# Optimization experiments

Hardware: AMD Instinct MI355X
Metric: run time of the kernel (lower is better)

Reference implementation:

```python
import math
import jax, jax.numpy as jnp
import numpy as np

B, N = 1, 512
C_S, C_Z, C_H, H, PQ, PV = 384, 128, 16, 12, 4, 8
CONCAT = H * C_Z + H * C_H + H * PV * 3 + H * PV  # 2112
W_C = math.sqrt(2.0 / (9.0 * PQ))
W_L = math.sqrt(1.0 / 3.0)


def setup_inputs() -> dict:
    key = jax.random.key(0)
    ks = jax.random.split(key, 16)
    sc = 0.02
    return {
        "s": jax.random.normal(ks[0], (B, N, C_S), jnp.float32),
        "z": jax.random.normal(ks[1], (B, N, N, C_Z), jnp.float32),
        "R": jax.random.normal(ks[2], (B, N, 3, 3), jnp.float32),
        "t": jax.random.normal(ks[3], (B, N, 3), jnp.float32),
        "mask": jnp.ones((B, N), dtype=bool),
        "Wqkv": jax.random.normal(ks[4], (C_S, 3 * H * C_H), jnp.float32) * sc,
        "Wqk_pts": jax.random.normal(ks[5], (C_S, 2 * H * PQ * 3), jnp.float32) * sc,
        "bqk_pts": jnp.zeros((2 * H * PQ * 3,), jnp.float32),
        "Wv_pts": jax.random.normal(ks[6], (C_S, H * PV * 3), jnp.float32) * sc,
        "bv_pts": jnp.zeros((H * PV * 3,), jnp.float32),
        "Wb": jax.random.normal(ks[7], (C_Z, H), jnp.float32) * sc,
        "bb": jnp.zeros((H,), jnp.float32),
        "gamma": jnp.full((H,), 0.541324854612918, jnp.float32),
        "Wfin": jax.random.normal(ks[8], (CONCAT, C_S), jnp.float32) * sc,
        "bfin": jnp.zeros((C_S,), jnp.float32),
    }


def _apply_rigid(R, t, pts):
    # R: [B,N,3,3], t: [B,N,3], pts: [B,N,H,P,3] -> global frame
    return jnp.einsum('bnxy,bnhpy->bnhpx', R, pts) + t[:, :, None, None, :]


def _invert_apply_rigid(R, t, pts):
    # R^T (pts - t)
    return jnp.einsum('bnyx,bnhpy->bnhpx', R, pts - t[:, :, None, None, :])


def reference(s, z, R, t, mask, Wqkv, Wqk_pts, bqk_pts, Wv_pts, bv_pts,
              Wb, bb, gamma, Wfin, bfin):
    b_, n_ = s.shape[0], s.shape[1]
    qkv = (s @ Wqkv).reshape(b_, n_, 3, H, C_H)
    q, k, v = qkv[:, :, 0], qkv[:, :, 1], qkv[:, :, 2]
    term1 = jnp.einsum('bihc,bjhc->bhij', q, k) / math.sqrt(C_H)
    term2 = jnp.transpose(z @ Wb + bb, (0, 3, 1, 2))  # [B,H,i,j]

    qk_pts = (s @ Wqk_pts + bqk_pts).reshape(b_, n_, 2, H, PQ, 3)
    q_pts, k_pts = qk_pts[:, :, 0], qk_pts[:, :, 1]
    qg = _apply_rigid(R, t, q_pts)  # [B,N,H,PQ,3]
    kg = _apply_rigid(R, t, k_pts)
    # squared distance summed over points and xyz -> [B,i,j,H]
    diff2 = jnp.sum((qg[:, :, None] - kg[:, None]) ** 2, axis=(-2, -1))
    term3 = (jax.nn.softplus(gamma)[None, :, None, None] * (W_C / 2.0)
             * jnp.transpose(diff2, (0, 3, 1, 2)))

    logits = W_L * (term1 + term2 - term3)
    logits = jnp.where(mask[:, None, None, :], logits, -1e9)
    aw = jax.nn.softmax(logits, axis=-1)  # [B,H,i,j]

    out_tilde = jnp.einsum('bhij,bijc->bihc', aw, z)
    out = jnp.einsum('bhij,bjhc->bihc', aw, v)

    v_pts = (s @ Wv_pts + bv_pts).reshape(b_, n_, H, PV, 3)
    vg = _apply_rigid(R, t, v_pts)
    o_global = jnp.einsum('bhij,bjhvx->bihvx', aw, vg)
    o_vec = _invert_apply_rigid(R, t, o_global)  # [B,N,H,PV,3]
    o_norm = jnp.sqrt(jnp.sum(o_vec ** 2, axis=-1) + 1e-8)

    feats = jnp.concatenate([
        out_tilde.reshape(b_, n_, -1),
        out.reshape(b_, n_, -1),
        o_vec.reshape(b_, n_, -1),
        o_norm.reshape(b_, n_, -1),
    ], axis=-1)
    return feats @ Wfin + bfin
```

## Files before the change

### kernel.cpp

```cpp
#include <hip/hip_runtime.h>
#include <math.h>

#define NSEQ 512
#define CS   384
#define NH   12
#define CHD  16
#define CZ   128
#define CONCATD 2112

#define W_L      0.57735026918962576f
#define W_C_HALF 0.117851130197757925f

typedef float f32x4 __attribute__((ext_vector_type(4)));
typedef short bf16x8 __attribute__((ext_vector_type(8)));
typedef unsigned int u32x2 __attribute__((ext_vector_type(2)));
typedef unsigned int u32x4 __attribute__((ext_vector_type(4)));

__device__ __forceinline__ unsigned short f2bf(float f) {
    union { float f; unsigned int u; } v; v.f = f;
    unsigned int u = v.u + 0x7FFFu + ((v.u >> 16) & 1u);
    return (unsigned short)(u >> 16);
}
__device__ __forceinline__ float bf2f(unsigned short u) {
    union { unsigned int i; float f; } v; v.i = ((unsigned int)u) << 16; return v.f;
}

#define MFMA16(A, B, C) __builtin_amdgcn_mfma_f32_16x16x32_bf16((A), (B), (C), 0, 0, 0)

#define RAWBAR() do {                                          \
    __builtin_amdgcn_sched_barrier(0);                         \
    asm volatile("s_waitcnt lgkmcnt(0)" ::: "memory");         \
    __builtin_amdgcn_s_barrier();                              \
    __builtin_amdgcn_sched_barrier(0);                         \
} while (0)

__global__ __launch_bounds__(256) void ipa_prep(
    const float* __restrict__ s, const float* __restrict__ Wqkv,
    const float* __restrict__ Wqk, const float* __restrict__ Wv,
    const float* __restrict__ bqk, const float* __restrict__ bv,
    const float* __restrict__ Wfin,
    unsigned short* __restrict__ sb, unsigned short* __restrict__ WcatT,
    float* __restrict__ biasv, unsigned short* __restrict__ WfinT)
{
    __shared__ float tile[32][33];
    if (blockIdx.x >= 314) {
        int b = blockIdx.x - 314;
        int kt = b / 12, nt = b - kt * 12;
        int k0 = kt * 32, n0 = nt * 32;
        #pragma unroll
        for (int it = 0; it < 4; ++it) {
            int idx = it * 256 + threadIdx.x;
            int ty = idx >> 5, tx = idx & 31;
            tile[ty][tx] = Wfin[(size_t)(k0 + ty) * 384 + n0 + tx];
        }
        __syncthreads();
        #pragma unroll
        for (int it = 0; it < 4; ++it) {
            int idx = it * 256 + threadIdx.x;
            int ty = idx >> 5, tx = idx & 31;
            WfinT[(size_t)(n0 + ty) * 2112 + k0 + tx] = f2bf(tile[tx][ty]);
        }
        return;
    }
    int v = blockIdx.x * 256 + threadIdx.x;
    if (v < 24576) {
        const float* src = s + (size_t)v * 8;
        f32x4 a = *(const f32x4*)src, b = *(const f32x4*)(src + 4);
        u32x4 pk;
        pk[0] = (unsigned)f2bf(a[0]) | ((unsigned)f2bf(a[1]) << 16);
        pk[1] = (unsigned)f2bf(a[2]) | ((unsigned)f2bf(a[3]) << 16);
        pk[2] = (unsigned)f2bf(b[0]) | ((unsigned)f2bf(b[1]) << 16);
        pk[3] = (unsigned)f2bf(b[2]) | ((unsigned)f2bf(b[3]) << 16);
        *(u32x4*)(sb + (size_t)v * 8) = pk;
    } else if (v < 79872) {
        int v2 = v - 24576;
        int n = v2 / 48;
        int kq = (v2 - n * 48) * 8;
        const float* W; int stride; int col; float sc = 1.f;
        if (n < 576)      { W = Wqkv; stride = 576; col = n;       if (n < 192) sc = 0.25f; }
        else if (n < 864) { W = Wqk;  stride = 288; col = n - 576; }
        else              { W = Wv;   stride = 288; col = n - 864; }
        const float* src = W + (size_t)kq * stride + col;
        unsigned int pk[4];
        #pragma unroll
        for (int e = 0; e < 4; ++e) {
            float v0 = src[(size_t)(2 * e) * stride] * sc;
            float v1 = src[(size_t)(2 * e + 1) * stride] * sc;
            pk[e] = (unsigned)f2bf(v0) | ((unsigned)f2bf(v1) << 16);
        }
        u32x4 pkv = {pk[0], pk[1], pk[2], pk[3]};
        *(u32x4*)(WcatT + (size_t)n * 384 + kq) = pkv;
    } else if (v < 80160) {
        int c0 = (v - 79872) * 4;
        #pragma unroll
        for (int e = 0; e < 4; ++e) {
            int c = c0 + e;
            biasv[c] = (c < 576) ? 0.f : ((c < 864) ? bqk[c - 576] : bv[c - 864]);
        }
    }
}

__global__ __launch_bounds__(256) void ipa_pg_t2(
    const unsigned short* __restrict__ sb, const unsigned short* __restrict__ WcatT,
    const float* __restrict__ biasv, float* __restrict__ proj,
    const float* __restrict__ z, const float* __restrict__ Wb,
    const float* __restrict__ bb, unsigned short* __restrict__ S)
{
    __shared__ __align__(16) char smem[26112];
    const int tid = threadIdx.x, lane = tid & 63, wv = tid >> 6;
    const int l15 = lane & 15, hi = lane >> 4;
    const int koff = hi * 8;
    const f32x4 ZV = {0.f, 0.f, 0.f, 0.f};

    if (blockIdx.x < 288) {
        const int n0 = ((int)blockIdx.x % 18) * 64;
        const int m0 = ((int)blockIdx.x / 18) * 32;
        unsigned short (*A_l)[136] = (unsigned short(*)[136])smem;
        unsigned short (*B_l)[136] = (unsigned short(*)[136])(smem + 8704);
        f32x4 C[4];
        #pragma unroll
        for (int nf = 0; nf < 4; ++nf) C[nf] = ZV;

        #pragma unroll
        for (int kc = 0; kc < 3; ++kc) {
            const int k0 = kc * 128;
            __syncthreads();
            #pragma unroll
            for (int it = 0; it < 2; ++it) {
                int v = it * 256 + tid;
                int row = v >> 4, c8 = v & 15;
                *(u32x4*)&A_l[row][c8 * 8] =
                    *(const u32x4*)(sb + (size_t)(m0 + row) * 384 + k0 + c8 * 8);
            }
            #pragma unroll
            for (int it = 0; it < 4; ++it) {
                int v = it * 256 + tid;
                int row = v >> 4, c8 = v & 15;
                *(u32x4*)&B_l[row][c8 * 8] =
                    *(const u32x4*)(WcatT + (size_t)(n0 + row) * 384 + k0 + c8 * 8);
            }
            __syncthreads();
            if (wv < 2) {
                #pragma unroll
                for (int ks = 0; ks < 4; ++ks) {
                    bf16x8 Af = *(const bf16x8*)&A_l[wv * 16 + l15][ks * 32 + koff];
                    #pragma unroll
                    for (int nf = 0; nf < 4; ++nf) {
                        bf16x8 Bf = *(const bf16x8*)&B_l[nf * 16 + l15][ks * 32 + koff];
                        C[nf] = MFMA16(Af, Bf, C[nf]);
                    }
                }
            }
        }
        if (wv < 2) {
            #pragma unroll
            for (int nf = 0; nf < 4; ++nf) {
                int col = n0 + nf * 16 + l15;
                float bval = biasv[col];
                #pragma unroll
                for (int r = 0; r < 4; ++r) {
                    int row = m0 + wv * 16 + hi * 4 + r;
                    proj[(size_t)row * 1152 + col] = C[nf][r] + bval;
                }
            }
        }
    } else {
        const int b = blockIdx.x - 288;
        const int i = b >> 3;
        const int j0 = (b & 7) * 64;
        unsigned short (*z_l)[136] = (unsigned short(*)[136])smem;

        bf16x8 wbf[4];
        #pragma unroll
        for (int ks = 0; ks < 4; ++ks) {
            bf16x8 rfr;
            #pragma unroll
            for (int e = 0; e < 8; ++e) {
                int c = ks * 32 + koff + e;
                float w = (l15 < 12) ? Wb[c * 12 + l15] : 0.f;
                rfr[e] = (short)f2bf(w);
            }
            wbf[ks] = rfr;
        }
        float bbv[4];
        #pragma unroll
        for (int r = 0; r < 4; ++r) { int h = hi * 4 + r; bbv[r] = (h < 12) ? bb[h] : 0.f; }

        #pragma unroll
        for (int it = 0; it < 4; ++it) {
            int u = it * 256 + tid;
            int row = u >> 4, c8 = u & 15;
            const float* src = z + ((size_t)(i * 512 + j0 + row)) * 128 + c8 * 8;
            f32x4 a = *(const f32x4*)src, bq = *(const f32x4*)(src + 4);
            u32x4 pk;
            pk[0] = (unsigned)f2bf(a[0]) | ((unsigned)f2bf(a[1]) << 16);
            pk[1] = (unsigned)f2bf(a[2]) | ((unsigned)f2bf(a[3]) << 16);
            pk[2] = (unsigned)f2bf(bq[0]) | ((unsigned)f2bf(bq[1]) << 16);
            pk[3] = (unsigned)f2bf(bq[2]) | ((unsigned)f2bf(bq[3]) << 16);
            *(u32x4*)&z_l[row][c8 * 8] = pk;
        }
        __syncthreads();

        const int jcol = wv * 16 + l15;
        f32x4 C = ZV;
        #pragma unroll
        for (int ks = 0; ks < 4; ++ks)
            C = MFMA16(wbf[ks], *(const bf16x8*)&z_l[jcol][ks * 32 + koff], C);
        #pragma unroll
        for (int r = 0; r < 4; ++r) {
            int h = hi * 4 + r;
            if (h < 12)
                S[(size_t)h * 262144 + (size_t)i * 512 + j0 + jcol] = f2bf(C[r] + bbv[r]);
        }
    }
}

__global__ __launch_bounds__(256) void ipa_projep(
    const float* __restrict__ proj, const float* __restrict__ R, const float* __restrict__ t,
    const float* __restrict__ gamma,
    unsigned short* __restrict__ Aaug, unsigned short* __restrict__ Baug,
    unsigned short* __restrict__ VcatT, float* __restrict__ rq, float* __restrict__ rk)
{
    const int half = threadIdx.x >> 7;
    const int i = blockIdx.x * 2 + half;
    const int st = threadIdx.x & 127;
    __shared__ float R_l[2][9], t_l[2][3], sq_l[2][96];
    __shared__ float sh_l[12];

    if (st < 9) R_l[half][st] = R[i * 9 + st];
    if (st >= 12 && st < 15) t_l[half][st - 12] = t[i * 3 + st - 12];
    if (threadIdx.x >= 240 && threadIdx.x < 252) {
        int h = threadIdx.x - 240;
        float spg = logf(1.f + __expf(gamma[h])) * W_C_HALF;
        sh_l[h] = sqrtf(2.f * spg);
    }
    __syncthreads();

    const float* row = proj + (size_t)i * 1152;

    for (int c = st; c < 576; c += 128) {
        unsigned short b16 = f2bf(row[c]);
        if (c < 192) {
            Aaug[((size_t)(c >> 4) * 512 + i) * 32 + (c & 15)] = b16;
        } else if (c < 384) {
            int cc = c - 192;
            Baug[((size_t)(cc >> 4) * 512 + i) * 32 + (cc & 15)] = b16;
        } else {
            int cc = c - 384;
            VcatT[((size_t)((cc >> 4) * 48 + (cc & 15))) * 512 + i] = b16;
        }
    }

    const float* Rr = R_l[half];
    const float* tt = t_l[half];
    for (int pt = st; pt < 192; pt += 128) {
        if (pt < 96) {
            int lp = (pt < 48) ? pt : pt - 48;
            int h = lp >> 2, p = lp & 3;
            int base = 576 + pt * 3;
            float p0 = row[base], p1 = row[base + 1], p2 = row[base + 2];
            float sh = sh_l[h];
            float g0 = (Rr[0] * p0 + Rr[1] * p1 + Rr[2] * p2 + tt[0]) * sh;
            float g1 = (Rr[3] * p0 + Rr[4] * p1 + Rr[5] * p2 + tt[1]) * sh;
            float g2 = (Rr[6] * p0 + Rr[7] * p1 + Rr[8] * p2 + tt[2]) * sh;
            sq_l[half][pt] = g0 * g0 + g1 * g1 + g2 * g2;
            unsigned short* dst =
                (pt < 48 ? Aaug : Baug) + ((size_t)h * 512 + i) * 32 + 16 + p * 3;
            dst[0] = f2bf(g0); dst[1] = f2bf(g1); dst[2] = f2bf(g2);
        } else {
            int vp = pt - 96;
            int h = vp >> 3, vv = vp & 7;
            int base = 864 + vp * 3;
            float p0 = row[base], p1 = row[base + 1], p2 = row[base + 2];
            float g0 = Rr[0] * p0 + Rr[1] * p1 + Rr[2] * p2 + tt[0];
            float g1 = Rr[3] * p0 + Rr[4] * p1 + Rr[5] * p2 + tt[1];
            float g2 = Rr[6] * p0 + Rr[7] * p1 + Rr[8] * p2 + tt[2];
            size_t rbase = ((size_t)h * 48 + 16 + vv * 3) * 512 + i;
            VcatT[rbase] = f2bf(g0);
            VcatT[rbase + 512] = f2bf(g1);
            VcatT[rbase + 1024] = f2bf(g2);
        }
    }
    __syncthreads();

    if (st < 24) {
        int qk = st / 12, h = st - qk * 12;
        int b0 = qk * 48 + h * 4;
        float ssum = sq_l[half][b0] + sq_l[half][b0 + 1]
                   + sq_l[half][b0 + 2] + sq_l[half][b0 + 3];
        (qk ? rk : rq)[h * 512 + i] = 0.5f * ssum;
    }
    if (st >= 32 && st < 56) {
        int e = st - 32;
        int mt = e / 12, h = e - mt * 12;
        *(unsigned long long*)((mt ? Baug : Aaug) + ((size_t)h * 512 + i) * 32 + 28) = 0ull;
    }
}

__global__ __launch_bounds__(256) void ipa_smax(
    const unsigned short* __restrict__ S, const unsigned short* __restrict__ Aaug,
    const unsigned short* __restrict__ Baug, const float* __restrict__ rq,
    const float* __restrict__ rk, unsigned short* __restrict__ P1, float* __restrict__ l1)
{
    const int h = blockIdx.x, i0 = blockIdx.y * 16;
    const int tid = threadIdx.x, lane = tid & 63, wv = tid >> 6;
    const int col = lane & 15, hi = lane >> 4;
    __shared__ __align__(16) unsigned short Baug_l[512][40];
    __shared__ __align__(16) unsigned short Aaug_l[16][40];
    __shared__ float rk_l[512], rq_l[16];
    __shared__ float pmx[4][16], psm[4][16];

    for (int u = tid; u < 2048; u += 256) {
        int row = u >> 2, seg = u & 3;
        *(u32x4*)&Baug_l[row][seg * 8] =
            *(const u32x4*)(Baug + ((size_t)h * 512 + row) * 32 + seg * 8);
    }
    if (tid < 64) {
        int row = tid >> 2, seg = tid & 3;
        *(u32x4*)&Aaug_l[row][seg * 8] =
            *(const u32x4*)(Aaug + ((size_t)h * 512 + i0 + row) * 32 + seg * 8);
    }
    for (int u = tid; u < 512; u += 256) rk_l[u] = rk[h * 512 + u];
    if (tid >= 64 && tid < 80) rq_l[tid - 64] = rq[h * 512 + i0 + tid - 64];
    __syncthreads();

    const f32x4 ZV = {0.f, 0.f, 0.f, 0.f};
    bf16x8 Af = *(const bf16x8*)&Aaug_l[col][hi * 8];
    f32x4 C[8];
    #pragma unroll
    for (int nf = 0; nf < 8; ++nf) {
        int n = wv * 8 + nf;
        bf16x8 Bf = *(const bf16x8*)&Baug_l[n * 16 + col][hi * 8];
        C[nf] = MFMA16(Af, Bf, ZV);
    }
    const unsigned short* Srow = S + (size_t)h * 262144 + (size_t)i0 * 512;
    float rmax[4] = {-1e30f, -1e30f, -1e30f, -1e30f};
    #pragma unroll
    for (int nf = 0; nf < 8; ++nf) {
        int j = wv * 128 + nf * 16 + col;
        float rkj = rk_l[j];
        #pragma unroll
        for (int r = 0; r < 4; ++r) {
            int il = hi * 4 + r;
            float Sv = bf2f(Srow[(size_t)il * 512 + j]);
            float L = W_L * (C[nf][r] + Sv - rq_l[il] - rkj);
            C[nf][r] = L;
            rmax[r] = fmaxf(rmax[r], L);
        }
    }
    #pragma unroll
    for (int o = 8; o; o >>= 1)
        #pragma unroll
        for (int r = 0; r < 4; ++r) rmax[r] = fmaxf(rmax[r], __shfl_xor(rmax[r], o));
    if (col == 0)
        #pragma unroll
        for (int r = 0; r < 4; ++r) pmx[wv][hi * 4 + r] = rmax[r];
    __syncthreads();
    float M[4], lsum[4] = {0.f, 0.f, 0.f, 0.f};
    #pragma unroll
    for (int r = 0; r < 4; ++r) {
        int il = hi * 4 + r;
        M[r] = fmaxf(fmaxf(pmx[0][il], pmx[1][il]), fmaxf(pmx[2][il], pmx[3][il]));
    }
    #pragma unroll
    for (int nf = 0; nf < 8; ++nf)
        #pragma unroll
        for (int r = 0; r < 4; ++r) {
            float p = __expf(C[nf][r] - M[r]);
            C[nf][r] = p;
            lsum[r] += p;
        }
    #pragma unroll
    for (int o = 8; o; o >>= 1)
        #pragma unroll
        for (int r = 0; r < 4; ++r) lsum[r] += __shfl_xor(lsum[r], o);
    if (col == 0)
        #pragma unroll
        for (int r = 0; r < 4; ++r) psm[wv][hi * 4 + r] = lsum[r];
    __syncthreads();
    if (wv == 0 && col == 0) {
        #pragma unroll
        for (int r = 0; r < 4; ++r) {
            int il = hi * 4 + r;
            l1[h * 512 + i0 + il] = psm[0][il] + psm[1][il] + psm[2][il] + psm[3][il];
        }
    }
    unsigned short* Prow = P1 + (size_t)h * 262144 + (size_t)i0 * 512;
    #pragma unroll
    for (int nf = 0; nf < 8; ++nf) {
        int j = wv * 128 + nf * 16 + col;
        #pragma unroll
        for (int r = 0; r < 4; ++r)
            Prow[(size_t)(hi * 4 + r) * 512 + j] = f2bf(C[nf][r]);
    }
}

__global__ __launch_bounds__(256) void ipa_otpv(
    const float* __restrict__ z, const unsigned short* __restrict__ P1,
    const float* __restrict__ l1, const unsigned short* __restrict__ VcatT,
    const float* __restrict__ R, const float* __restrict__ t,
    unsigned short* __restrict__ featsb)
{
    __shared__ __align__(16) char smem[35072];
    const int tid = threadIdx.x, lane = tid & 63, wv = tid >> 6;
    const int l15 = lane & 15, hi = lane >> 4;
    const int koff = hi * 8;
    const f32x4 ZV = {0.f, 0.f, 0.f, 0.f};

    if (blockIdx.x < 1024) {
        const int i = blockIdx.x >> 1;
        const int chalf = ((int)blockIdx.x & 1) * 64;
        unsigned short (*P_l)[520] = (unsigned short(*)[520])smem;
        typedef unsigned short zt_t[64][72];
        zt_t* zT = (zt_t*)(smem + 16640);

        for (int u = tid; u < 1024; u += 256) {
            int row = u >> 6, c8 = u & 63;
            *(u32x4*)&P_l[row][c8 * 8] =
                *(const u32x4*)(P1 + (size_t)row * 262144 + (size_t)i * 512 + c8 * 8);
        }
        __syncthreads();

        f32x4 sa[4];
        #pragma unroll
        for (int it = 0; it < 4; ++it) {
            int u = it * 256 + tid;
            int jj = u >> 4, c4l = u & 15;
            sa[it] = *(const f32x4*)(z + ((size_t)(i * 512 + jj)) * 128 + chalf + c4l * 4);
        }

        f32x4 Co = ZV;
        for (int jt = 0; jt < 8; ++jt) {
            const int cur = jt & 1;
            #pragma unroll
            for (int it = 0; it < 4; ++it) {
                int u = it * 256 + tid;
                int jj = u >> 4, c4l = u & 15;
                f32x4 zv = sa[it];
                unsigned short b0 = f2bf(zv[0]), b1 = f2bf(zv[1]), b2 = f2bf(zv[2]), b3 = f2bf(zv[3]);
                unsigned int w01 = (unsigned)b0 | ((unsigned)b1 << 16);
                unsigned int w23 = (unsigned)b2 | ((unsigned)b3 << 16);
                unsigned int p01 = (unsigned int)__shfl_xor((int)w01, 16);
                unsigned int p23 = (unsigned int)__shfl_xor((int)w23, 16);
                bool even = ((tid & 16) == 0);
                unsigned short q0 = (unsigned short)(p01 & 0xffff), q1 = (unsigned short)(p01 >> 16);
                unsigned short q2 = (unsigned short)(p23 & 0xffff), q3 = (unsigned short)(p23 >> 16);
                unsigned int w0, w1, w2, w3;
                if (even) {
                    w0 = (unsigned)b0 | ((unsigned)q0 << 16); w1 = (unsigned)b1 | ((unsigned)q1 << 16);
                    w2 = (unsigned)b2 | ((unsigned)q2 << 16); w3 = (unsigned)b3 | ((unsigned)q3 << 16);
                } else {
                    w0 = (unsigned)q0 | ((unsigned)b0 << 16); w1 = (unsigned)q1 | ((unsigned)b1 << 16);
                    w2 = (unsigned)q2 | ((unsigned)b2 << 16); w3 = (unsigned)q3 | ((unsigned)b3 << 16);
                }
                int jp = jj >> 1;
                int rot = ((c4l >> 1) & 3) + (even ? 0 : 2);
                #pragma unroll
                for (int ss = 0; ss < 2; ++ss) {
                    int rr = (rot + ss) & 3;
                    unsigned int val = (rr == 0) ? w0 : ((rr == 1) ? w1 : ((rr == 2) ? w2 : w3));
                    *(unsigned int*)&zT[cur][4 * c4l + rr][2 * jp] = val;
                }
            }
            if (jt < 7) {
                const int j0n = (jt + 1) * 64;
                #pragma unroll
                for (int it = 0; it < 4; ++it) {
                    int u = it * 256 + tid;
                    int jj = u >> 4, c4l = u & 15;
                    sa[it] = *(const f32x4*)(z + ((size_t)(i * 512 + j0n + jj)) * 128 + chalf + c4l * 4);
                }
            }
            RAWBAR();
            #pragma unroll
            for (int ks2 = 0; ks2 < 2; ++ks2) {
                bf16x8 Af = *(const bf16x8*)&P_l[l15][jt * 64 + ks2 * 32 + koff];
                bf16x8 Bf = *(const bf16x8*)&zT[cur][wv * 16 + l15][ks2 * 32 + koff];
                Co = MFMA16(Af, Bf, Co);
            }
        }

        #pragma unroll
        for (int r = 0; r < 4; ++r) {
            int h = hi * 4 + r;
            if (h < 12)
                featsb[(size_t)i * CONCATD + h * 128 + chalf + wv * 16 + l15]
                    = f2bf(Co[r] / l1[h * 512 + i]);
        }
    } else {
        const int b = blockIdx.x - 1024;
        const int h = b >> 3, i0 = (b & 7) * 64;
        const int col = l15;
        unsigned short (*V_l)[264] = (unsigned short(*)[264])smem;
        float (*ogl)[26] = (float(*)[26])(smem + 25344);

        f32x4 C0 = ZV, C1 = ZV, C2 = ZV;
        const unsigned short* Pbase =
            P1 + (size_t)h * 262144 + (size_t)(i0 + wv * 16 + col) * 512;
        #pragma unroll
        for (int hf = 0; hf < 2; ++hf) {
            __syncthreads();
            for (int u = tid; u < 1536; u += 256) {
                int row = u >> 5, c8 = u & 31;
                *(u32x4*)&V_l[row][c8 * 8] =
                    *(const u32x4*)(VcatT + ((size_t)h * 48 + row) * 512 + hf * 256 + c8 * 8);
            }
            __syncthreads();
            #pragma unroll
            for (int ks2 = 0; ks2 < 8; ++ks2) {
                bf16x8 Af = *(const bf16x8*)(Pbase + hf * 256 + ks2 * 32 + hi * 8);
                C0 = MFMA16(Af, *(const bf16x8*)&V_l[col][ks2 * 32 + hi * 8],      C0);
                C1 = MFMA16(Af, *(const bf16x8*)&V_l[16 + col][ks2 * 32 + hi * 8], C1);
                C2 = MFMA16(Af, *(const bf16x8*)&V_l[32 + col][ks2 * 32 + hi * 8], C2);
            }
        }
        #pragma unroll
        for (int r = 0; r < 4; ++r) {
            int il = wv * 16 + hi * 4 + r;
            int irow = i0 + il;
            float inv = 1.f / l1[h * 512 + irow];
            featsb[(size_t)irow * CONCATD + 1536 + h * 16 + col] = f2bf(C0[r] * inv);
            ogl[il][col] = C1[r] * inv;
            if (col < 8) ogl[il][16 + col] = C2[r] * inv;
        }
        __syncthreads();

        #pragma unroll
        for (int it = 0; it < 2; ++it) {
            int item = it * 256 + tid;
            int il = item >> 3, v = item & 7;
            int i = i0 + il;
            const float* Rr = R + i * 9;
            const float* tt = t + i * 3;
            float g0 = ogl[il][v * 3 + 0] - tt[0];
            float g1 = ogl[il][v * 3 + 1] - tt[1];
            float g2 = ogl[il][v * 3 + 2] - tt[2];
            float o0 = Rr[0] * g0 + Rr[3] * g1 + Rr[6] * g2;
            float o1 = Rr[1] * g0 + Rr[4] * g1 + Rr[7] * g2;
            float o2 = Rr[2] * g0 + Rr[5] * g1 + Rr[8] * g2;
            unsigned short* frow = featsb + (size_t)i * CONCATD;
            frow[1728 + h * 24 + v * 3 + 0] = f2bf(o0);
            frow[1728 + h * 24 + v * 3 + 1] = f2bf(o1);
            frow[1728 + h * 24 + v * 3 + 2] = f2bf(o2);
            frow[2016 + h * 8 + v] = f2bf(sqrtf(o0 * o0 + o1 * o1 + o2 * o2 + 1e-8f));
        }
    }
}

__global__ __launch_bounds__(128) void ipa_finalb(
    const unsigned short* __restrict__ featsb, const unsigned short* __restrict__ WfinT,
    float* __restrict__ fpart)
{
    const int n0 = blockIdx.x * 64, m0 = blockIdx.y * 32;
    const int k0 = blockIdx.z * 192;
    const int tid = threadIdx.x, lane = tid & 63, wv = tid >> 6;
    const int l15 = lane & 15, hi = lane >> 4;
    __shared__ __align__(16) unsigned short A_l[32][200];
    __shared__ __align__(16) unsigned short B_l[64][200];

    #pragma unroll
    for (int it = 0; it < 6; ++it) {
        int v = it * 128 + tid;
        int row = v / 24, c8 = v % 24;
        *(u32x4*)&A_l[row][c8 * 8] =
            *(const u32x4*)(featsb + (size_t)(m0 + row) * CONCATD + k0 + c8 * 8);
    }
    #pragma unroll
    for (int it = 0; it < 12; ++it) {
        int v = it * 128 + tid;
        int row = v / 24, c8 = v % 24;
        *(u32x4*)&B_l[row][c8 * 8] =
            *(const u32x4*)(WfinT + (size_t)(n0 + row) * 2112 + k0 + c8 * 8);
    }
    __syncthreads();

    const f32x4 ZV = {0.f, 0.f, 0.f, 0.f};
    f32x4 C[4];
    #pragma unroll
    for (int nf = 0; nf < 4; ++nf) C[nf] = ZV;
    const int koff = hi * 8;
    #pragma unroll
    for (int ks = 0; ks < 6; ++ks) {
        bf16x8 Af = *(const bf16x8*)&A_l[wv * 16 + l15][ks * 32 + koff];
        #pragma unroll
        for (int nf = 0; nf < 4; ++nf) {
            bf16x8 Bf = *(const bf16x8*)&B_l[nf * 16 + l15][ks * 32 + koff];
            C[nf] = MFMA16(Af, Bf, C[nf]);
        }
    }
    float* P = fpart + (size_t)blockIdx.z * (NSEQ * CS);
    #pragma unroll
    for (int nf = 0; nf < 4; ++nf) {
        int colx = n0 + nf * 16 + l15;
        #pragma unroll
        for (int r = 0; r < 4; ++r) {
            int row = m0 + wv * 16 + hi * 4 + r;
            P[(size_t)row * CS + colx] = C[nf][r];
        }
    }
}

__global__ __launch_bounds__(256) void ipa_reduceb(
    const float* __restrict__ fpart, const float* __restrict__ bias, float* __restrict__ out)
{
    int idx = blockIdx.x * 256 + threadIdx.x;
    f32x4 acc = ((const f32x4*)bias)[idx % (CS / 4)];
    #pragma unroll
    for (int kc = 0; kc < 11; ++kc)
        acc += ((const f32x4*)(fpart + (size_t)kc * (NSEQ * CS)))[idx];
    ((f32x4*)out)[idx] = acc;
}

extern "C" void kernel_launch(void* const* d_in, const int* in_sizes, int n_in,
                              void* d_out, int out_size, void* d_ws, size_t ws_size,
                              hipStream_t stream) {
    (void)in_sizes; (void)n_in; (void)out_size; (void)ws_size;
    const float* s    = (const float*)d_in[0];
    const float* z    = (const float*)d_in[1];
    const float* R    = (const float*)d_in[2];
    const float* t    = (const float*)d_in[3];
    const float* Wqkv = (const float*)d_in[5];
    const float* Wqk  = (const float*)d_in[6];
    const float* bqk  = (const float*)d_in[7];
    const float* Wv   = (const float*)d_in[8];
    const float* bv   = (const float*)d_in[9];
    const float* Wb   = (const float*)d_in[10];
    const float* bb   = (const float*)d_in[11];
    const float* gam  = (const float*)d_in[12];
    const float* Wfin = (const float*)d_in[13];
    const float* bfin = (const float*)d_in[14];
    float* out = (float*)d_out;

    char* w8 = (char*)d_ws;
    unsigned short* S     = (unsigned short*)(w8 + 0);
    unsigned short* P1    = (unsigned short*)(w8 + 6291456);
    unsigned short* featsb= (unsigned short*)(w8 + 12582912);
    unsigned short* WfinT = (unsigned short*)(w8 + 14745600);
    unsigned short* Aaug  = (unsigned short*)(w8 + 16908288);
    unsigned short* Baug  = (unsigned short*)(w8 + 17301504);
    unsigned short* VcatT = (unsigned short*)(w8 + 17694720);
    float* rq             = (float*)(w8 + 18284544);
    float* rk             = (float*)(w8 + 18309120);
    float* l1             = (float*)(w8 + 18333696);
    float* fpart          = (float*)(w8 + 0);
    float* proj           = (float*)(w8 + 6291456 + 2359296);
    unsigned short* sb    = (unsigned short*)(w8 + 2359296);
    unsigned short* WcatT = (unsigned short*)(w8 + 2752512);
    float* biasv          = (float*)(w8 + 3637248);

    sb    = (unsigned short*)(w8 + 12582912);
    WcatT = (unsigned short*)(w8 + 12582912 + 393216);
    biasv = (float*)(w8 + 12582912 + 1277952);

    ipa_prep<<<1106, 256, 0, stream>>>(s, Wqkv, Wqk, Wv, bqk, bv, Wfin,
                                       sb, WcatT, biasv, WfinT);
    ipa_pg_t2<<<4384, 256, 0, stream>>>(sb, WcatT, biasv, proj, z, Wb, bb, S);
    ipa_projep<<<256, 256, 0, stream>>>(proj, R, t, gam, Aaug, Baug, VcatT, rq, rk);
    ipa_smax<<<dim3(12, 32), 256, 0, stream>>>(S, Aaug, Baug, rq, rk, P1, l1);
    ipa_otpv<<<1120, 256, 0, stream>>>(z, P1, l1, VcatT, R, t, featsb);
    ipa_finalb<<<dim3(6, 16, 11), 128, 0, stream>>>(featsb, WfinT, fpart);
    ipa_reduceb<<<192, 256, 0, stream>>>(fpart, bfin, out);
}
```

Baseline: 84.84 us.

## Fuse prep conversion kernel into projection/z-bias kernel, converting weights on the fly

Removes the separate prep launch by having the projection GEMM blocks convert s and the Wqkv/Wqk/Wv weights from fp32 to bf16 while loading tiles. The weight tile is transposed in registers with lane shuffles and stored into LDS. The bias is read directly from the inputs instead of a staged buffer. The Wfin transpose moves into the same launch as extra blocks. This saves one kernel launch and the intermediate global round-trip, at the cost of redundant fp32 loads and conversion work in each GEMM block.

```diff
diff --git a/kernel.cpp b/kernel.cpp
--- a/kernel.cpp
+++ b/kernel.cpp
@@ -34,77 +34,14 @@
     __builtin_amdgcn_sched_barrier(0);                         \
 } while (0)
 
-__global__ __launch_bounds__(256) void ipa_prep(
+__global__ __launch_bounds__(256) void ipa_l1(
+    const float* __restrict__ z, const float* __restrict__ Wb,
+    const float* __restrict__ bb, unsigned short* __restrict__ S,
     const float* __restrict__ s, const float* __restrict__ Wqkv,
     const float* __restrict__ Wqk, const float* __restrict__ Wv,
     const float* __restrict__ bqk, const float* __restrict__ bv,
-    const float* __restrict__ Wfin,
-    unsigned short* __restrict__ sb, unsigned short* __restrict__ WcatT,
-    float* __restrict__ biasv, unsigned short* __restrict__ WfinT)
-{
-    __shared__ float tile[32][33];
-    if (blockIdx.x >= 314) {
-        int b = blockIdx.x - 314;
-        int kt = b / 12, nt = b - kt * 12;
-        int k0 = kt * 32, n0 = nt * 32;
-        #pragma unroll
-        for (int it = 0; it < 4; ++it) {
-            int idx = it * 256 + threadIdx.x;
-            int ty = idx >> 5, tx = idx & 31;
-            tile[ty][tx] = Wfin[(size_t)(k0 + ty) * 384 + n0 + tx];
-        }
-        __syncthreads();
-        #pragma unroll
-        for (int it = 0; it < 4; ++it) {
-            int idx = it * 256 + threadIdx.x;
-            int ty = idx >> 5, tx = idx & 31;
-            WfinT[(size_t)(n0 + ty) * 2112 + k0 + tx] = f2bf(tile[tx][ty]);
-        }
-        return;
-    }
-    int v = blockIdx.x * 256 + threadIdx.x;
-    if (v < 24576) {
-        const float* src = s + (size_t)v * 8;
-        f32x4 a = *(const f32x4*)src, b = *(const f32x4*)(src + 4);
-        u32x4 pk;
-        pk[0] = (unsigned)f2bf(a[0]) | ((unsigned)f2bf(a[1]) << 16);
-        pk[1] = (unsigned)f2bf(a[2]) | ((unsigned)f2bf(a[3]) << 16);
-        pk[2] = (unsigned)f2bf(b[0]) | ((unsigned)f2bf(b[1]) << 16);
-        pk[3] = (unsigned)f2bf(b[2]) | ((unsigned)f2bf(b[3]) << 16);
-        *(u32x4*)(sb + (size_t)v * 8) = pk;
-    } else if (v < 79872) {
-        int v2 = v - 24576;
-        int n = v2 / 48;
-        int kq = (v2 - n * 48) * 8;
-        const float* W; int stride; int col; float sc = 1.f;
-        if (n < 576)      { W = Wqkv; stride = 576; col = n;       if (n < 192) sc = 0.25f; }
-        else if (n < 864) { W = Wqk;  stride = 288; col = n - 576; }
-        else              { W = Wv;   stride = 288; col = n - 864; }
-        const float* src = W + (size_t)kq * stride + col;
-        unsigned int pk[4];
-        #pragma unroll
-        for (int e = 0; e < 4; ++e) {
-            float v0 = src[(size_t)(2 * e) * stride] * sc;
-            float v1 = src[(size_t)(2 * e + 1) * stride] * sc;
-            pk[e] = (unsigned)f2bf(v0) | ((unsigned)f2bf(v1) << 16);
-        }
-        u32x4 pkv = {pk[0], pk[1], pk[2], pk[3]};
-        *(u32x4*)(WcatT + (size_t)n * 384 + kq) = pkv;
-    } else if (v < 80160) {
-        int c0 = (v - 79872) * 4;
-        #pragma unroll
-        for (int e = 0; e < 4; ++e) {
-            int c = c0 + e;
-            biasv[c] = (c < 576) ? 0.f : ((c < 864) ? bqk[c - 576] : bv[c - 864]);
-        }
-    }
-}
-
-__global__ __launch_bounds__(256) void ipa_pg_t2(
-    const unsigned short* __restrict__ sb, const unsigned short* __restrict__ WcatT,
-    const float* __restrict__ biasv, float* __restrict__ proj,
-    const float* __restrict__ z, const float* __restrict__ Wb,
-    const float* __restrict__ bb, unsigned short* __restrict__ S)
+    float* __restrict__ proj,
+    const float* __restrict__ Wfin, unsigned short* __restrict__ WfinT)
 {
     __shared__ __align__(16) char smem[26112];
     const int tid = threadIdx.x, lane = tid & 63, wv = tid >> 6;
@@ -112,9 +49,58 @@
     const int koff = hi * 8;
     const f32x4 ZV = {0.f, 0.f, 0.f, 0.f};
 
-    if (blockIdx.x < 288) {
-        const int n0 = ((int)blockIdx.x % 18) * 64;
-        const int m0 = ((int)blockIdx.x / 18) * 32;
+    if (blockIdx.x < 4096) {
+        const int b = blockIdx.x;
+        const int i = b >> 3;
+        const int j0 = (b & 7) * 64;
+        unsigned short (*z_l)[136] = (unsigned short(*)[136])smem;
+
+        bf16x8 wbf[4];
+        #pragma unroll
+        for (int ks = 0; ks < 4; ++ks) {
+            bf16x8 rfr;
+            #pragma unroll
+            for (int e = 0; e < 8; ++e) {
+                int c = ks * 32 + koff + e;
+                float w = (l15 < 12) ? Wb[c * 12 + l15] : 0.f;
+                rfr[e] = (short)f2bf(w);
+            }
+            wbf[ks] = rfr;
+        }
+        float bbv[4];
+        #pragma unroll
+        for (int r = 0; r < 4; ++r) { int h = hi * 4 + r; bbv[r] = (h < 12) ? bb[h] : 0.f; }
+
+        #pragma unroll
+        for (int it = 0; it < 4; ++it) {
+            int u = it * 256 + tid;
+            int row = u >> 4, c8 = u & 15;
+            const float* src = z + ((size_t)(i * 512 + j0 + row)) * 128 + c8 * 8;
+            f32x4 a = *(const f32x4*)src, bq = *(const f32x4*)(src + 4);
+            u32x4 pk;
+            pk[0] = (unsigned)f2bf(a[0]) | ((unsigned)f2bf(a[1]) << 16);
+            pk[1] = (unsigned)f2bf(a[2]) | ((unsigned)f2bf(a[3]) << 16);
+            pk[2] = (unsigned)f2bf(bq[0]) | ((unsigned)f2bf(bq[1]) << 16);
+            pk[3] = (unsigned)f2bf(bq[2]) | ((unsigned)f2bf(bq[3]) << 16);
+            *(u32x4*)&z_l[row][c8 * 8] = pk;
+        }
+        __syncthreads();
+
+        const int jcol = wv * 16 + l15;
+        f32x4 C = ZV;
+        #pragma unroll
+        for (int ks = 0; ks < 4; ++ks)
+            C = MFMA16(wbf[ks], *(const bf16x8*)&z_l[jcol][ks * 32 + koff], C);
+        #pragma unroll
+        for (int r = 0; r < 4; ++r) {
+            int h = hi * 4 + r;
+            if (h < 12)
+                S[(size_t)h * 262144 + (size_t)i * 512 + j0 + jcol] = f2bf(C[r] + bbv[r]);
+        }
+    } else if (blockIdx.x < 4384) {
+        const int b = blockIdx.x - 4096;
+        const int n0 = (b % 18) * 64;
+        const int m0 = (b / 18) * 32;
         unsigned short (*A_l)[136] = (unsigned short(*)[136])smem;
         unsigned short (*B_l)[136] = (unsigned short(*)[136])(smem + 8704);
         f32x4 C[4];
@@ -127,17 +113,57 @@
             __syncthreads();
             #pragma unroll
             for (int it = 0; it < 2; ++it) {
-                int v = it * 256 + tid;
-                int row = v >> 4, c8 = v & 15;
-                *(u32x4*)&A_l[row][c8 * 8] =
-                    *(const u32x4*)(sb + (size_t)(m0 + row) * 384 + k0 + c8 * 8);
+                int u = it * 256 + tid;
+                int row = u >> 4, c8 = u & 15;
+                const float* src = s + (size_t)(m0 + row) * 384 + k0 + c8 * 8;
+                f32x4 a = *(const f32x4*)src, bq = *(const f32x4*)(src + 4);
+                u32x4 pk;
+                pk[0] = (unsigned)f2bf(a[0]) | ((unsigned)f2bf(a[1]) << 16);
+                pk[1] = (unsigned)f2bf(a[2]) | ((unsigned)f2bf(a[3]) << 16);
+                pk[2] = (unsigned)f2bf(bq[0]) | ((unsigned)f2bf(bq[1]) << 16);
+                pk[3] = (unsigned)f2bf(bq[2]) | ((unsigned)f2bf(bq[3]) << 16);
+                *(u32x4*)&A_l[row][c8 * 8] = pk;
             }
             #pragma unroll
-            for (int it = 0; it < 4; ++it) {
-                int v = it * 256 + tid;
-                int row = v >> 4, c8 = v & 15;
-                *(u32x4*)&B_l[row][c8 * 8] =
-                    *(const u32x4*)(WcatT + (size_t)(n0 + row) * 384 + k0 + c8 * 8);
+            for (int kh = 0; kh < 2; ++kh) {
+                #pragma unroll
+                for (int it = 0; it < 4; ++it) {
+                    int u = it * 256 + tid;
+                    int kk = u >> 4, c4l = u & 15;
+                    int n = n0 + 4 * c4l;
+                    int k = k0 + kh * 64 + kk;
+                    const float* Wp; int ncols, coln; float sc = 1.f;
+                    if (n < 576)      { Wp = Wqkv; ncols = 576; coln = n;       if (n < 192) sc = 0.25f; }
+                    else if (n < 864) { Wp = Wqk;  ncols = 288; coln = n - 576; }
+                    else              { Wp = Wv;   ncols = 288; coln = n - 864; }
+                    f32x4 wval = *(const f32x4*)(Wp + (size_t)k * ncols + coln);
+                    wval *= sc;
+                    unsigned short b0 = f2bf(wval[0]), b1 = f2bf(wval[1]);
+                    unsigned short b2 = f2bf(wval[2]), b3 = f2bf(wval[3]);
+                    unsigned int w01 = (unsigned)b0 | ((unsigned)b1 << 16);
+                    unsigned int w23 = (unsigned)b2 | ((unsigned)b3 << 16);
+                    unsigned int p01 = (unsigned int)__shfl_xor((int)w01, 16);
+                    unsigned int p23 = (unsigned int)__shfl_xor((int)w23, 16);
+                    bool even = ((tid & 16) == 0);
+                    unsigned short q0 = (unsigned short)(p01 & 0xffff), q1 = (unsigned short)(p01 >> 16);
+                    unsigned short q2 = (unsigned short)(p23 & 0xffff), q3 = (unsigned short)(p23 >> 16);
+                    unsigned int w0, w1, w2, w3;
+                    if (even) {
+                        w0 = (unsigned)b0 | ((unsigned)q0 << 16); w1 = (unsigned)b1 | ((unsigned)q1 << 16);
+                        w2 = (unsigned)b2 | ((unsigned)q2 << 16); w3 = (unsigned)b3 | ((unsigned)q3 << 16);
+                    } else {
+                        w0 = (unsigned)q0 | ((unsigned)b0 << 16); w1 = (unsigned)q1 | ((unsigned)b1 << 16);
+                        w2 = (unsigned)q2 | ((unsigned)b2 << 16); w3 = (unsigned)q3 | ((unsigned)b3 << 16);
+                    }
+                    int jp = kk >> 1;
+                    int rot = ((c4l >> 1) & 3) + (even ? 0 : 2);
+                    #pragma unroll
+                    for (int ss = 0; ss < 2; ++ss) {
+                        int rr = (rot + ss) & 3;
+                        unsigned int val = (rr == 0) ? w0 : ((rr == 1) ? w1 : ((rr == 2) ? w2 : w3));
+                        *(unsigned int*)&B_l[4 * c4l + rr][kh * 64 + 2 * jp] = val;
+                    }
+                }
             }
             __syncthreads();
             if (wv < 2) {
@@ -156,7 +182,8 @@
             #pragma unroll
             for (int nf = 0; nf < 4; ++nf) {
                 int col = n0 + nf * 16 + l15;
-                float bval = biasv[col];
+                float bval = (col < 576) ? 0.f
+                           : ((col < 864) ? bqk[col - 576] : bv[col - 864]);
                 #pragma unroll
                 for (int r = 0; r < 4; ++r) {
                     int row = m0 + wv * 16 + hi * 4 + r;
@@ -165,52 +192,22 @@
             }
         }
     } else {
-        const int b = blockIdx.x - 288;
-        const int i = b >> 3;
-        const int j0 = (b & 7) * 64;
-        unsigned short (*z_l)[136] = (unsigned short(*)[136])smem;
-
-        bf16x8 wbf[4];
-        #pragma unroll
-        for (int ks = 0; ks < 4; ++ks) {
-            bf16x8 rfr;
-            #pragma unroll
-            for (int e = 0; e < 8; ++e) {
-                int c = ks * 32 + koff + e;
-                float w = (l15 < 12) ? Wb[c * 12 + l15] : 0.f;
-                rfr[e] = (short)f2bf(w);
-            }
-            wbf[ks] = rfr;
-        }
-        float bbv[4];
-        #pragma unroll
-        for (int r = 0; r < 4; ++r) { int h = hi * 4 + r; bbv[r] = (h < 12) ? bb[h] : 0.f; }
-
+        int b = blockIdx.x - 4384;
+        int kt = b / 12, nt = b - kt * 12;
+        int k0 = kt * 32, n0 = nt * 32;
+        float (*tile)[33] = (float(*)[33])smem;
         #pragma unroll
         for (int it = 0; it < 4; ++it) {
-            int u = it * 256 + tid;
-            int row = u >> 4, c8 = u & 15;
-            const float* src = z + ((size_t)(i * 512 + j0 + row)) * 128 + c8 * 8;
-            f32x4 a = *(const f32x4*)src, bq = *(const f32x4*)(src + 4);
-            u32x4 pk;
-            pk[0] = (unsigned)f2bf(a[0]) | ((unsigned)f2bf(a[1]) << 16);
-            pk[1] = (unsigned)f2bf(a[2]) | ((unsigned)f2bf(a[3]) << 16);
-            pk[2] = (unsigned)f2bf(bq[0]) | ((unsigned)f2bf(bq[1]) << 16);
-            pk[3] = (unsigned)f2bf(bq[2]) | ((unsigned)f2bf(bq[3]) << 16);
-            *(u32x4*)&z_l[row][c8 * 8] = pk;
+            int idx = it * 256 + tid;
+            int ty = idx >> 5, tx = idx & 31;
+            tile[ty][tx] = Wfin[(size_t)(k0 + ty) * 384 + n0 + tx];
         }
         __syncthreads();
-
-        const int jcol = wv * 16 + l15;
-        f32x4 C = ZV;
-        #pragma unroll
-        for (int ks = 0; ks < 4; ++ks)
-            C = MFMA16(wbf[ks], *(const bf16x8*)&z_l[jcol][ks * 32 + koff], C);
-        #pragma unroll
-        for (int r = 0; r < 4; ++r) {
-            int h = hi * 4 + r;
-            if (h < 12)
-                S[(size_t)h * 262144 + (size_t)i * 512 + j0 + jcol] = f2bf(C[r] + bbv[r]);
+        #pragma unroll
+        for (int it = 0; it < 4; ++it) {
+            int idx = it * 256 + tid;
+            int ty = idx >> 5, tx = idx & 31;
+            WfinT[(size_t)(n0 + ty) * 2112 + k0 + tx] = f2bf(tile[tx][ty]);
         }
     }
 }
@@ -644,17 +641,10 @@
     float* l1             = (float*)(w8 + 18333696);
     float* fpart          = (float*)(w8 + 0);
     float* proj           = (float*)(w8 + 6291456 + 2359296);
-    unsigned short* sb    = (unsigned short*)(w8 + 2359296);
-    unsigned short* WcatT = (unsigned short*)(w8 + 2752512);
-    float* biasv          = (float*)(w8 + 3637248);
-
-    sb    = (unsigned short*)(w8 + 12582912);
-    WcatT = (unsigned short*)(w8 + 12582912 + 393216);
-    biasv = (float*)(w8 + 12582912 + 1277952);
-
-    ipa_prep<<<1106, 256, 0, stream>>>(s, Wqkv, Wqk, Wv, bqk, bv, Wfin,
-                                       sb, WcatT, biasv, WfinT);
-    ipa_pg_t2<<<4384, 256, 0, stream>>>(sb, WcatT, biasv, proj, z, Wb, bb, S);
+
+    ipa_l1<<<5176, 256, 0, stream>>>(z, Wb, bb, S,
+                                     s, Wqkv, Wqk, Wv, bqk, bv, proj,
+                                     Wfin, WfinT);
     ipa_projep<<<256, 256, 0, stream>>>(proj, R, t, gam, Aaug, Baug, VcatT, rq, rk);
     ipa_smax<<<dim3(12, 32), 256, 0, stream>>>(S, Aaug, Baug, rq, rk, P1, l1);
     ipa_otpv<<<1120, 256, 0, stream>>>(z, P1, l1, VcatT, R, t, featsb);
```

Result: slower. 91.40 us (+7.7%).
